# Performance work log

Measured on AMD Instinct MI355X. Metric: run time of the kernel, lower is better.

The kernel has to match this reference:

```python
import jax, jax.numpy as jnp
import numpy as np

B, S, F = 4, 2048, 512
H, DK, DV, FILT = 8, 64, 64, 512

def setup_inputs() -> dict:
    key = jax.random.key(0)
    ks = jax.random.split(key, 11)
    sc_in = 1.0 / np.sqrt(F)
    sc_o = 1.0 / np.sqrt(H * DV)
    return {
        "x_q": jax.random.normal(ks[0], (B, S, F), jnp.float32),
        "x_k": jax.random.normal(ks[1], (B, S, F), jnp.float32),
        "x_v": jax.random.normal(ks[2], (B, S, F), jnp.float32),
        "Wq": jax.random.normal(ks[3], (H, F, DK), jnp.float32) * sc_in,
        "bq": jax.random.normal(ks[4], (H, DK), jnp.float32) * 0.01,
        "Wk": jax.random.normal(ks[5], (H, F, DK), jnp.float32) * sc_in,
        "bk": jax.random.normal(ks[6], (H, DK), jnp.float32) * 0.01,
        "Wv": jax.random.normal(ks[7], (H, F, DV), jnp.float32) * sc_in,
        "bv": jax.random.normal(ks[8], (H, DV), jnp.float32) * 0.01,
        "Wo": jax.random.normal(ks[9], (H * DV, FILT), jnp.float32) * sc_o,
        "bo": jax.random.normal(ks[10], (FILT,), jnp.float32) * 0.01,
    }

def reference(x_q, x_k, x_v, Wq, bq, Wk, bk, Wv, bv, Wo, bo):
    d_k = Wq.shape[-1]
    # per-head Dense projections, batched over heads: [B,H,S,dk/dv]
    q = jnp.einsum("bsf,hfk->bhsk", x_q, Wq) + bq[:, None, :]
    k = jnp.einsum("bsf,hfk->bhsk", x_k, Wk) + bk[:, None, :]
    v = jnp.einsum("bsf,hfv->bhsv", x_v, Wv) + bv[:, None, :]
    # scaled dot-product attention (scale by 1/sqrt(d_k) as in map_fn)
    scores = jnp.einsum("bhsk,bhtk->bhst", q, k) / jnp.sqrt(jnp.asarray(d_k, q.dtype))
    attn = jax.nn.softmax(scores, axis=-1)
    out = jnp.einsum("bhst,bhtv->bhsv", attn, v)
    # concat heads along feature dim -> [B,S,H*DV], then output linear
    bsz, h, s, dv = out.shape
    concat = out.transpose(0, 2, 1, 3).reshape(bsz, s, h * dv)
    return concat @ Wo + bo
```

## Files before the change

kernel.cpp:

```cpp
#include <hip/hip_runtime.h>

#define B_    4
#define S_    2048
#define H_    8
#define M_    (B_ * S_)

typedef __bf16    bf16_t;
typedef _Float16  f16_t;
typedef __bf16   bf16x8 __attribute__((ext_vector_type(8)));
typedef __bf16   bf16x4 __attribute__((ext_vector_type(4)));
typedef _Float16 f16x8  __attribute__((ext_vector_type(8)));
typedef float    f32x16 __attribute__((ext_vector_type(16)));

union B8 { uint4 u; bf16x8 v; bf16_t e[8]; };
union B4 { uint2 u; bf16x4 v; bf16_t e[4]; };
union H8 { uint4 u; f16x8  v; f16_t  e[8]; };
union H4 { uint2 u; f16_t  e[4]; };

#define QSCALE 0.1803368801111204f

typedef const __attribute__((address_space(1))) unsigned int ga_u32;
typedef __attribute__((address_space(3))) unsigned int       ls_u32;
__device__ __forceinline__ void g2l16(const void* g, void* l) {
    __builtin_amdgcn_global_load_lds((ga_u32*)g, (ls_u32*)l, 16, 0, 0);
}

__global__ __launch_bounds__(256) void cast_x(
    const float* __restrict__ xq, const float* __restrict__ xk,
    const float* __restrict__ xv,
    bf16_t* __restrict__ dq, bf16_t* __restrict__ dk, bf16_t* __restrict__ dv)
{
    const int z = blockIdx.y;
    const float* src = z == 0 ? xq : z == 1 ? xk : xv;
    bf16_t*      dst = z == 0 ? dq : z == 1 ? dk : dv;
    const size_t base = (size_t)blockIdx.x * 4096 + threadIdx.x * 4;
    #pragma unroll
    for (int k = 0; k < 4; ++k) {
        const size_t i = base + (size_t)k * 1024;
        float4 v = *(const float4*)(src + i);
        B4 o;
        o.e[0] = (bf16_t)v.x; o.e[1] = (bf16_t)v.y;
        o.e[2] = (bf16_t)v.z; o.e[3] = (bf16_t)v.w;
        *(uint2*)(dst + i) = o.u;
    }
}

__global__ __launch_bounds__(256) void convert_weights(
    const float* __restrict__ w0, const float* __restrict__ w1,
    const float* __restrict__ w2, const float* __restrict__ wo,
    bf16_t* __restrict__ t0, bf16_t* __restrict__ t1,
    bf16_t* __restrict__ t2, f16_t* __restrict__ wot)
{
    __shared__ float T[64][65];
    const int z   = blockIdx.z;
    const int k0  = blockIdx.x * 64;
    const int tid = threadIdx.x;
    const int row = tid & 63, q4 = tid >> 6;

    if (z < 3) {
        const float* W  = z == 0 ? w0 : z == 1 ? w1 : w2;
        bf16_t*      Wt = z == 0 ? t0 : z == 1 ? t1 : t2;
        const int h = blockIdx.y;
        const float* Wh = W + (size_t)h * 512 * 64;
        #pragma unroll
        for (int i = 0; i < 4; ++i) {
            int fq = q4 * 4 + i;
            float4 v = *(const float4*)(Wh + (size_t)(k0 + row) * 64 + fq * 4);
            T[row][fq * 4 + 0] = v.x; T[row][fq * 4 + 1] = v.y;
            T[row][fq * 4 + 2] = v.z; T[row][fq * 4 + 3] = v.w;
        }
        __syncthreads();
        bf16_t* Wth = Wt + (size_t)h * 64 * 512;
        #pragma unroll
        for (int i = 0; i < 4; ++i) {
            int kq = q4 * 4 + i;
            B4 o;
            #pragma unroll
            for (int j = 0; j < 4; ++j) o.e[j] = (bf16_t)T[kq * 4 + j][row];
            *(uint2*)(Wth + (size_t)row * 512 + k0 + kq * 4) = o.u;
        }
    } else {
        const int n0 = blockIdx.y * 64;
        #pragma unroll
        for (int i = 0; i < 4; ++i) {
            int fq = q4 * 4 + i;
            float4 v = *(const float4*)(wo + (size_t)(k0 + row) * 512 + n0 + fq * 4);
            T[row][fq * 4 + 0] = v.x; T[row][fq * 4 + 1] = v.y;
            T[row][fq * 4 + 2] = v.z; T[row][fq * 4 + 3] = v.w;
        }
        __syncthreads();
        #pragma unroll
        for (int i = 0; i < 4; ++i) {
            int kq = q4 * 4 + i;
            H4 o;
            #pragma unroll
            for (int j = 0; j < 4; ++j) o.e[j] = (f16_t)T[kq * 4 + j][row];
            *(uint2*)(wot + (size_t)(n0 + row) * 512 + k0 + kq * 4) = o.u;
        }
    }
}

__global__ __launch_bounds__(256) void proj_tiled(
    const bf16_t* __restrict__ xq, const bf16_t* __restrict__ xk,
    const bf16_t* __restrict__ xv,
    const bf16_t* __restrict__ Wtq, const bf16_t* __restrict__ Wtk,
    const bf16_t* __restrict__ Wtv,
    const float* __restrict__ bq, const float* __restrict__ bk,
    const float* __restrict__ bv,
    bf16_t* __restrict__ Qb, bf16_t* __restrict__ Kb, bf16_t* __restrict__ Vt)
{
    __shared__ char sm[34816];
    bf16_t* As = (bf16_t*)sm;
    bf16_t* Bs = As + 128 * 64;

    const int z = blockIdx.z;
    const bf16_t* X    = z == 0 ? xq  : z == 1 ? xk  : xv;
    const bf16_t* Wt   = z == 0 ? Wtq : z == 1 ? Wtk : Wtv;
    const float*  bias = z == 0 ? bq  : z == 1 ? bk  : bv;

    const int tid  = threadIdx.x;
    const int wave = tid >> 6, lane = tid & 63;
    const int l31  = lane & 31, half = lane >> 5;
    const int m0   = blockIdx.x * 128;
    const int n0   = blockIdx.y * 128;
    const int mw   = (wave & 1) * 64;
    const int nw   = (wave >> 1) * 64;

    const int srow = lane >> 3;
    const int scol = (lane & 7) * 16;

    f32x16 acc[2][2];
    #pragma unroll
    for (int mt = 0; mt < 2; ++mt)
        #pragma unroll
        for (int nt = 0; nt < 2; ++nt)
            #pragma unroll
            for (int i = 0; i < 16; ++i) acc[mt][nt][i] = 0.0f;

    for (int k0 = 0; k0 < 512; k0 += 64) {
        __syncthreads();
        #pragma unroll
        for (int i = 0; i < 4; ++i) {
            const int inst = wave * 4 + i;
            const int row  = inst * 8 + srow;
            g2l16((const char*)X  + ((size_t)(m0 + row) * 512 + k0) * 2 + scol,
                  sm + inst * 1024);
            g2l16((const char*)Wt + ((size_t)(n0 + row) * 512 + k0) * 2 + scol,
                  sm + 16384 + inst * 1024);
        }
        __syncthreads();

        #pragma unroll
        for (int kc = 0; kc < 4; ++kc) {
            B8 a0, a1, b0, b1;
            a0.u = *(const uint4*)&As[(mw + l31)      * 64 + kc * 16 + half * 8];
            a1.u = *(const uint4*)&As[(mw + 32 + l31) * 64 + kc * 16 + half * 8];
            b0.u = *(const uint4*)&Bs[(nw + l31)      * 64 + kc * 16 + half * 8];
            b1.u = *(const uint4*)&Bs[(nw + 32 + l31) * 64 + kc * 16 + half * 8];
            acc[0][0] = __builtin_amdgcn_mfma_f32_32x32x16_bf16(a0.v, b0.v, acc[0][0], 0, 0, 0);
            acc[0][1] = __builtin_amdgcn_mfma_f32_32x32x16_bf16(a0.v, b1.v, acc[0][1], 0, 0, 0);
            acc[1][0] = __builtin_amdgcn_mfma_f32_32x32x16_bf16(a1.v, b0.v, acc[1][0], 0, 0, 0);
            acc[1][1] = __builtin_amdgcn_mfma_f32_32x32x16_bf16(a1.v, b1.v, acc[1][1], 0, 0, 0);
        }
    }

    if (z <= 1) {
        const float sc_ = (z == 0) ? QSCALE : 1.0f;
        bf16_t* Out = (z == 0) ? Qb : Kb;
        #pragma unroll
        for (int mt = 0; mt < 2; ++mt)
            #pragma unroll
            for (int nt = 0; nt < 2; ++nt) {
                int n = n0 + nw + nt * 32 + l31;
                float bv_ = bias[n];
                #pragma unroll
                for (int r = 0; r < 16; ++r) {
                    int m = m0 + mw + mt * 32 + (r & 3) + 8 * (r >> 2) + 4 * half;
                    Out[(size_t)m * 512 + n] = (bf16_t)((acc[mt][nt][r] + bv_) * sc_);
                }
            }
    } else {
        const int b  = m0 >> 11;
        const int sb = m0 & 2047;
        __syncthreads();
        #pragma unroll
        for (int mt = 0; mt < 2; ++mt)
            #pragma unroll
            for (int nt = 0; nt < 2; ++nt) {
                const int nl  = nw + nt * 32 + l31;
                const float bv_ = bias[n0 + nl];
                #pragma unroll
                for (int r = 0; r < 16; r += 2) {
                    const int ml = mw + mt * 32 + (r & 3) + 8 * (r >> 2) + 4 * half;
                    union { unsigned u; bf16_t e[2]; } pk;
                    pk.e[0] = (bf16_t)(acc[mt][nt][r]     + bv_);
                    pk.e[1] = (bf16_t)(acc[mt][nt][r + 1] + bv_);
                    *(unsigned*)(sm + nl * 272 + ml * 2) = pk.u;
                }
            }
        __syncthreads();
        const int dl16 = tid >> 4;
        const int cc   = tid & 15;
        #pragma unroll
        for (int p = 0; p < 8; ++p) {
            const int d_l = p * 16 + dl16;
            const int ng  = n0 + d_l;
            const int h   = ng >> 6, dd = ng & 63;
            uint4 val = *(const uint4*)(sm + d_l * 272 + cc * 16);
            *(uint4*)(Vt + ((size_t)((b * 8 + h) * 64 + dd)) * 2048 + sb + cc * 8) = val;
        }
    }
}

__global__ __launch_bounds__(512) void attn_mfma(
    const bf16_t* __restrict__ Q, const bf16_t* __restrict__ K,
    const bf16_t* __restrict__ Vt, f16_t* __restrict__ O)
{
    __shared__ char smraw[36864];
    bf16_t* KsBuf = (bf16_t*)smraw;
    bf16_t* VsBuf = KsBuf + 2 * 64 * 72;

    const int bh  = blockIdx.y;
    const int b   = bh >> 3, h = bh & 7;
    const int q0  = blockIdx.x * 128;
    const int tid = threadIdx.x;
    const int wave = tid >> 6, lane = tid & 63;
    const int l31 = lane & 31, half = lane >> 5;
    const int qsub = wave & 3, ksplit = wave >> 2;

    bf16x8 qf[4];
    {
        const bf16_t* qp = Q + ((size_t)(b * S_ + q0 + qsub * 32 + l31)) * 512 + h * 64 + half * 8;
        #pragma unroll
        for (int ks = 0; ks < 4; ++ks) {
            B8 t; t.u = *(const uint4*)(qp + ks * 16);
            qf[ks] = t.v;
        }
    }

    f32x16 o0, o1;
    #pragma unroll
    for (int i = 0; i < 16; ++i) { o0[i] = 0.0f; o1[i] = 0.0f; }
    float l_i = 0.0f;

    const bf16_t* Kbase = K + ((size_t)b * S_) * 512 + h * 64;
    const bf16_t* Vbase = Vt + ((size_t)bh * 64) * 2048;

    const int sbuf = tid >> 8;
    const int p    = tid & 255;
    const int kr = p >> 3, kc8 = p & 7;
    const int vd = p >> 2, vj = p & 3;
    const int kqmap[4] = {0, 2, 1, 3};
    const int vkq = kqmap[vj];
    bf16_t* KsS = KsBuf + sbuf * (64 * 72);
    bf16_t* VsS = VsBuf + sbuf * (64 * 72);
    const bf16_t* KsC = KsBuf + ksplit * (64 * 72);
    const bf16_t* VsC = VsBuf + ksplit * (64 * 72);

    uint4 kreg0, kreg1;
    uint2 vreg[4];
    {
        const int tb = sbuf * 1024;
        kreg0 = *(const uint4*)(Kbase + (size_t)(tb + kr) * 512 + kc8 * 8);
        kreg1 = *(const uint4*)(Kbase + (size_t)(tb + kr + 32) * 512 + kc8 * 8);
        #pragma unroll
        for (int g = 0; g < 4; ++g)
            vreg[g] = *(const uint2*)(Vbase + (size_t)vd * 2048 + tb + g * 16 + vkq * 4);
    }

    for (int t0 = 0; t0 < 1024; t0 += 64) {
        __syncthreads();
        *(uint4*)&KsS[kr * 72 + kc8 * 8]        = kreg0;
        *(uint4*)&KsS[(kr + 32) * 72 + kc8 * 8] = kreg1;
        #pragma unroll
        for (int g = 0; g < 4; ++g)
            *(uint2*)&VsS[vd * 72 + g * 16 + vj * 4] = vreg[g];
        __syncthreads();

        if (t0 + 64 < 1024) {
            const int tb = sbuf * 1024 + t0 + 64;
            kreg0 = *(const uint4*)(Kbase + (size_t)(tb + kr) * 512 + kc8 * 8);
            kreg1 = *(const uint4*)(Kbase + (size_t)(tb + kr + 32) * 512 + kc8 * 8);
            #pragma unroll
            for (int g = 0; g < 4; ++g)
                vreg[g] = *(const uint2*)(Vbase + (size_t)vd * 2048 + tb + g * 16 + vkq * 4);
        }

        f32x16 s0, s1;
        #pragma unroll
        for (int i = 0; i < 16; ++i) { s0[i] = 0.0f; s1[i] = 0.0f; }
        #pragma unroll
        for (int ks = 0; ks < 4; ++ks) {
            B8 k0, k1;
            k0.u = *(const uint4*)(&KsC[l31 * 72 + ks * 16 + half * 8]);
            k1.u = *(const uint4*)(&KsC[(32 + l31) * 72 + ks * 16 + half * 8]);
            s0 = __builtin_amdgcn_mfma_f32_32x32x16_bf16(k0.v, qf[ks], s0, 0, 0, 0);
            s1 = __builtin_amdgcn_mfma_f32_32x32x16_bf16(k1.v, qf[ks], s1, 0, 0, 0);
        }

        float ls = 0.0f;
        #pragma unroll
        for (int r = 0; r < 16; ++r) {
            s0[r] = __builtin_amdgcn_exp2f(s0[r]); ls += s0[r];
            s1[r] = __builtin_amdgcn_exp2f(s1[r]); ls += s1[r];
        }
        l_i += ls;

        B8 pf[4];
        #pragma unroll
        for (int j = 0; j < 8; ++j) {
            pf[0].e[j] = (bf16_t)s0[j];
            pf[1].e[j] = (bf16_t)s0[8 + j];
            pf[2].e[j] = (bf16_t)s1[j];
            pf[3].e[j] = (bf16_t)s1[8 + j];
        }

        #pragma unroll
        for (int c = 0; c < 4; ++c) {
            B8 va, vb;
            va.u = *(const uint4*)(&VsC[l31 * 72 + c * 16 + half * 8]);
            vb.u = *(const uint4*)(&VsC[(32 + l31) * 72 + c * 16 + half * 8]);
            o0 = __builtin_amdgcn_mfma_f32_32x32x16_bf16(va.v, pf[c].v, o0, 0, 0, 0);
            o1 = __builtin_amdgcn_mfma_f32_32x32x16_bf16(vb.v, pf[c].v, o1, 0, 0, 0);
        }
    }

    l_i += __shfl_xor(l_i, 32);
    __syncthreads();
    float* co = (float*)smraw;
    float* cl = co + 4 * 32 * 68;
    if (ksplit == 1) {
        float* reg = co + qsub * (32 * 68);
        #pragma unroll
        for (int r = 0; r < 16; ++r) {
            reg[r * 68 + lane]        = o0[r];
            reg[(16 + r) * 68 + lane] = o1[r];
        }
        cl[qsub * 64 + lane] = l_i;
    }
    __syncthreads();
    if (ksplit == 0) {
        float* reg = co + qsub * (32 * 68);
        float inv = 1.0f / (l_i + cl[qsub * 64 + lane]);
        f16_t* Ob = O + ((size_t)(b * S_ + q0 + qsub * 32 + l31)) * 512 + h * 64;
        #pragma unroll
        for (int g = 0; g < 4; ++g) {
            H4 a, c;
            #pragma unroll
            for (int j = 0; j < 4; ++j) {
                int r = g * 4 + j;
                a.e[j] = (f16_t)((o0[r] + reg[r * 68 + lane]) * inv);
                c.e[j] = (f16_t)((o1[r] + reg[(16 + r) * 68 + lane]) * inv);
            }
            int d = 8 * g + 4 * half;
            *(uint2*)(Ob + d)      = a.u;
            *(uint2*)(Ob + 32 + d) = c.u;
        }
    }
}

__global__ __launch_bounds__(256) void gemm_out_tiled(
    const f16_t* __restrict__ A, const f16_t* __restrict__ Wot,
    const float* __restrict__ bias, float* __restrict__ C)
{
    __shared__ f16_t As[64 * 72];
    __shared__ f16_t Bs[64 * 72];

    const int tid  = threadIdx.x;
    const int wave = tid >> 6, lane = tid & 63;
    const int l31  = lane & 31, half = lane >> 5;
    const int m0   = blockIdx.x * 64;
    const int n0   = blockIdx.y * 64;
    const int mw   = (wave & 1) * 32;
    const int nw   = (wave >> 1) * 32;

    const int sr  = tid >> 2;
    const int so  = (tid & 3) * 16;

    uint4 pA0, pA1, pB0, pB1;
    {
        const f16_t* ap = A   + (size_t)(m0 + sr) * 512 + so;
        const f16_t* bp = Wot + (size_t)(n0 + sr) * 512 + so;
        pA0 = *(const uint4*)(ap); pA1 = *(const uint4*)(ap + 8);
        pB0 = *(const uint4*)(bp); pB1 = *(const uint4*)(bp + 8);
    }

    f32x16 acc;
    #pragma unroll
    for (int i = 0; i < 16; ++i) acc[i] = 0.0f;

    for (int k0 = 0; k0 < 512; k0 += 64) {
        __syncthreads();
        *(uint4*)&As[sr * 72 + so]     = pA0;
        *(uint4*)&As[sr * 72 + so + 8] = pA1;
        *(uint4*)&Bs[sr * 72 + so]     = pB0;
        *(uint4*)&Bs[sr * 72 + so + 8] = pB1;
        __syncthreads();
        if (k0 + 64 < 512) {
            const f16_t* ap = A   + (size_t)(m0 + sr) * 512 + k0 + 64 + so;
            const f16_t* bp = Wot + (size_t)(n0 + sr) * 512 + k0 + 64 + so;
            pA0 = *(const uint4*)(ap); pA1 = *(const uint4*)(ap + 8);
            pB0 = *(const uint4*)(bp); pB1 = *(const uint4*)(bp + 8);
        }

        #pragma unroll
        for (int kc = 0; kc < 4; ++kc) {
            H8 a, b;
            a.u = *(const uint4*)&As[(mw + l31) * 72 + kc * 16 + half * 8];
            b.u = *(const uint4*)&Bs[(nw + l31) * 72 + kc * 16 + half * 8];
            acc = __builtin_amdgcn_mfma_f32_32x32x16_f16(a.v, b.v, acc, 0, 0, 0);
        }
    }

    const int n = n0 + nw + l31;
    const float bias0 = bias[n];
    #pragma unroll
    for (int r = 0; r < 16; ++r) {
        int m = m0 + mw + (r & 3) + 8 * (r >> 2) + 4 * half;
        C[(size_t)m * 512 + n] = acc[r] + bias0;
    }
}

extern "C" void kernel_launch(void* const* d_in, const int* in_sizes, int n_in,
                              void* d_out, int out_size, void* d_ws, size_t ws_size,
                              hipStream_t stream)
{
    const float* x_q = (const float*)d_in[0];
    const float* x_k = (const float*)d_in[1];
    const float* x_v = (const float*)d_in[2];
    const float* Wq  = (const float*)d_in[3];
    const float* bq  = (const float*)d_in[4];
    const float* Wk  = (const float*)d_in[5];
    const float* bk  = (const float*)d_in[6];
    const float* Wv  = (const float*)d_in[7];
    const float* bv  = (const float*)d_in[8];
    const float* Wo  = (const float*)d_in[9];
    const float* bo  = (const float*)d_in[10];
    float* out = (float*)d_out;

    char* W = (char*)d_ws;
    bf16_t* Wtq = (bf16_t*)W;
    bf16_t* Wtk = Wtq + (size_t)8 * 64 * 512;
    bf16_t* Wtv = Wtk + (size_t)8 * 64 * 512;
    f16_t*  Wot = (f16_t*)(Wtv + (size_t)8 * 64 * 512);
    bf16_t* Qb  = (bf16_t*)(Wot + (size_t)512 * 512);
    bf16_t* Kb  = Qb + (size_t)M_ * 512;
    bf16_t* Vt  = Kb + (size_t)M_ * 512;
    f16_t*  AO  = (f16_t*)(Vt + (size_t)M_ * 512);

    bf16_t* Xqb = (bf16_t*)out;
    bf16_t* Xkb = Xqb + (size_t)M_ * 512;
    bf16_t* Xvb = (bf16_t*)AO;

    cast_x<<<dim3(1024, 3), 256, 0, stream>>>(x_q, x_k, x_v, Xqb, Xkb, Xvb);

    convert_weights<<<dim3(8, 8, 4), 256, 0, stream>>>(
        Wq, Wk, Wv, Wo, Wtq, Wtk, Wtv, Wot);

    proj_tiled<<<dim3(64, 4, 3), 256, 0, stream>>>(
        Xqb, Xkb, Xvb, Wtq, Wtk, Wtv, bq, bk, bv, Qb, Kb, Vt);

    attn_mfma<<<dim3(S_ / 128, B_ * H_), 512, 0, stream>>>(Qb, Kb, Vt, AO);

    gemm_out_tiled<<<dim3(128, 8), 256, 0, stream>>>(AO, Wot, bo, out);
}
```

Before: 202.8 us.

## Double-buffer K/V register prefetch, remap blocks to head-major order, add MFMA priority

After: 199.1 us. No clear change (-1.8%).

```diff
diff --git a/kernel.cpp b/kernel.cpp
--- a/kernel.cpp
+++ b/kernel.cpp
@@ -220,9 +220,10 @@
     bf16_t* KsBuf = (bf16_t*)smraw;
     bf16_t* VsBuf = KsBuf + 2 * 64 * 72;
 
-    const int bh  = blockIdx.y;
+    const int lin = (int)(blockIdx.x + gridDim.x * blockIdx.y);
+    const int bh  = ((lin >> 7) << 3) + (lin & 7);
+    const int q0  = ((lin >> 3) & 15) * 128;
     const int b   = bh >> 3, h = bh & 7;
-    const int q0  = blockIdx.x * 128;
     const int tid = threadIdx.x;
     const int wave = tid >> 6, lane = tid & 63;
     const int l31 = lane & 31, half = lane >> 5;
@@ -257,38 +258,45 @@
     const bf16_t* KsC = KsBuf + ksplit * (64 * 72);
     const bf16_t* VsC = VsBuf + ksplit * (64 * 72);
 
-    uint4 kreg0, kreg1;
-    uint2 vreg[4];
-    {
-        const int tb = sbuf * 1024;
-        kreg0 = *(const uint4*)(Kbase + (size_t)(tb + kr) * 512 + kc8 * 8);
-        kreg1 = *(const uint4*)(Kbase + (size_t)(tb + kr + 32) * 512 + kc8 * 8);
-        #pragma unroll
-        for (int g = 0; g < 4; ++g)
-            vreg[g] = *(const uint2*)(Vbase + (size_t)vd * 2048 + tb + g * 16 + vkq * 4);
-    }
-
-    for (int t0 = 0; t0 < 1024; t0 += 64) {
-        __syncthreads();
-        *(uint4*)&KsS[kr * 72 + kc8 * 8]        = kreg0;
-        *(uint4*)&KsS[(kr + 32) * 72 + kc8 * 8] = kreg1;
-        #pragma unroll
-        for (int g = 0; g < 4; ++g)
-            *(uint2*)&VsS[vd * 72 + g * 16 + vj * 4] = vreg[g];
-        __syncthreads();
-
-        if (t0 + 64 < 1024) {
-            const int tb = sbuf * 1024 + t0 + 64;
-            kreg0 = *(const uint4*)(Kbase + (size_t)(tb + kr) * 512 + kc8 * 8);
-            kreg1 = *(const uint4*)(Kbase + (size_t)(tb + kr + 32) * 512 + kc8 * 8);
-            #pragma unroll
-            for (int g = 0; g < 4; ++g)
-                vreg[g] = *(const uint2*)(Vbase + (size_t)vd * 2048 + tb + g * 16 + vkq * 4);
+    uint4 k0A, k1A, k0B, k1B;
+    uint2 vA[4], vB[4];
+
+#define LOADSET(K0, K1, VV, TB) do {                                          \
+        K0 = *(const uint4*)(Kbase + (size_t)((TB) + kr) * 512 + kc8 * 8);    \
+        K1 = *(const uint4*)(Kbase + (size_t)((TB) + kr + 32) * 512 + kc8 * 8);\
+        _Pragma("unroll")                                                     \
+        for (int g = 0; g < 4; ++g)                                           \
+            VV[g] = *(const uint2*)(Vbase + (size_t)vd * 2048 + (TB) + g * 16 + vkq * 4); \
+    } while (0)
+
+#define WRITESET(K0, K1, VV) do {                                             \
+        *(uint4*)&KsS[kr * 72 + kc8 * 8]        = K0;                         \
+        *(uint4*)&KsS[(kr + 32) * 72 + kc8 * 8] = K1;                         \
+        _Pragma("unroll")                                                     \
+        for (int g = 0; g < 4; ++g)                                           \
+            *(uint2*)&VsS[vd * 72 + g * 16 + vj * 4] = VV[g];                 \
+    } while (0)
+
+    LOADSET(k0A, k1A, vA, sbuf * 1024);
+    LOADSET(k0B, k1B, vB, sbuf * 1024 + 64);
+
+    #pragma unroll
+    for (int it = 0; it < 16; ++it) {
+        __syncthreads();
+        if ((it & 1) == 0) WRITESET(k0A, k1A, vA);
+        else               WRITESET(k0B, k1B, vB);
+        __syncthreads();
+
+        if (it + 2 < 16) {
+            const int tb = sbuf * 1024 + it * 64 + 128;
+            if ((it & 1) == 0) LOADSET(k0A, k1A, vA, tb);
+            else               LOADSET(k0B, k1B, vB, tb);
         }
 
         f32x16 s0, s1;
         #pragma unroll
         for (int i = 0; i < 16; ++i) { s0[i] = 0.0f; s1[i] = 0.0f; }
+        __builtin_amdgcn_s_setprio(1);
         #pragma unroll
         for (int ks = 0; ks < 4; ++ks) {
             B8 k0, k1;
@@ -297,6 +305,7 @@
             s0 = __builtin_amdgcn_mfma_f32_32x32x16_bf16(k0.v, qf[ks], s0, 0, 0, 0);
             s1 = __builtin_amdgcn_mfma_f32_32x32x16_bf16(k1.v, qf[ks], s1, 0, 0, 0);
         }
+        __builtin_amdgcn_s_setprio(0);
 
         float ls = 0.0f;
         #pragma unroll
@@ -315,6 +324,7 @@
             pf[3].e[j] = (bf16_t)s1[8 + j];
         }
 
+        __builtin_amdgcn_s_setprio(1);
         #pragma unroll
         for (int c = 0; c < 4; ++c) {
             B8 va, vb;
@@ -323,7 +333,10 @@
             o0 = __builtin_amdgcn_mfma_f32_32x32x16_bf16(va.v, pf[c].v, o0, 0, 0, 0);
             o1 = __builtin_amdgcn_mfma_f32_32x32x16_bf16(vb.v, pf[c].v, o1, 0, 0, 0);
         }
-    }
+        __builtin_amdgcn_s_setprio(0);
+    }
+#undef LOADSET
+#undef WRITESET
 
     l_i += __shfl_xor(l_i, 32);
     __syncthreads();
```

## Process two query sub-tiles per wave in attention to reuse K/V tiles

Applied to the files above, without the earlier changes.

New measurement: 195.0 us. -3.8%, faster.

```diff
diff --git a/kernel.cpp b/kernel.cpp
--- a/kernel.cpp
+++ b/kernel.cpp
@@ -212,36 +212,37 @@
     }
 }
 
-__global__ __launch_bounds__(512) void attn_mfma(
+__global__ __launch_bounds__(512, 2) void attn_mfma(
     const bf16_t* __restrict__ Q, const bf16_t* __restrict__ K,
     const bf16_t* __restrict__ Vt, f16_t* __restrict__ O)
 {
-    __shared__ char smraw[36864];
+    __shared__ char smraw[71680];
     bf16_t* KsBuf = (bf16_t*)smraw;
     bf16_t* VsBuf = KsBuf + 2 * 64 * 72;
 
     const int bh  = blockIdx.y;
     const int b   = bh >> 3, h = bh & 7;
-    const int q0  = blockIdx.x * 128;
+    const int q0  = blockIdx.x * 256;
     const int tid = threadIdx.x;
     const int wave = tid >> 6, lane = tid & 63;
     const int l31 = lane & 31, half = lane >> 5;
     const int qsub = wave & 3, ksplit = wave >> 2;
 
-    bf16x8 qf[4];
+    bf16x8 qfA[4], qfB[4];
     {
-        const bf16_t* qp = Q + ((size_t)(b * S_ + q0 + qsub * 32 + l31)) * 512 + h * 64 + half * 8;
+        const bf16_t* qp = Q + ((size_t)(b * S_ + q0 + qsub * 64 + l31)) * 512 + h * 64 + half * 8;
         #pragma unroll
         for (int ks = 0; ks < 4; ++ks) {
-            B8 t; t.u = *(const uint4*)(qp + ks * 16);
-            qf[ks] = t.v;
-        }
-    }
-
-    f32x16 o0, o1;
+            B8 t;
+            t.u = *(const uint4*)(qp + ks * 16);              qfA[ks] = t.v;
+            t.u = *(const uint4*)(qp + 32 * 512 + ks * 16);   qfB[ks] = t.v;
+        }
+    }
+
+    f32x16 oA0, oA1, oB0, oB1;
     #pragma unroll
-    for (int i = 0; i < 16; ++i) { o0[i] = 0.0f; o1[i] = 0.0f; }
-    float l_i = 0.0f;
+    for (int i = 0; i < 16; ++i) { oA0[i] = 0.0f; oA1[i] = 0.0f; oB0[i] = 0.0f; oB1[i] = 0.0f; }
+    float lA = 0.0f, lB = 0.0f;
 
     const bf16_t* Kbase = K + ((size_t)b * S_) * 512 + h * 64;
     const bf16_t* Vbase = Vt + ((size_t)bh * 64) * 2048;
@@ -286,33 +287,41 @@
                 vreg[g] = *(const uint2*)(Vbase + (size_t)vd * 2048 + tb + g * 16 + vkq * 4);
         }
 
-        f32x16 s0, s1;
-        #pragma unroll
-        for (int i = 0; i < 16; ++i) { s0[i] = 0.0f; s1[i] = 0.0f; }
+        f32x16 s00, s01, s10, s11;
+        #pragma unroll
+        for (int i = 0; i < 16; ++i) { s00[i] = 0.0f; s01[i] = 0.0f; s10[i] = 0.0f; s11[i] = 0.0f; }
         #pragma unroll
         for (int ks = 0; ks < 4; ++ks) {
-            B8 k0, k1;
-            k0.u = *(const uint4*)(&KsC[l31 * 72 + ks * 16 + half * 8]);
-            k1.u = *(const uint4*)(&KsC[(32 + l31) * 72 + ks * 16 + half * 8]);
-            s0 = __builtin_amdgcn_mfma_f32_32x32x16_bf16(k0.v, qf[ks], s0, 0, 0, 0);
-            s1 = __builtin_amdgcn_mfma_f32_32x32x16_bf16(k1.v, qf[ks], s1, 0, 0, 0);
-        }
-
-        float ls = 0.0f;
+            B8 kk0, kk1;
+            kk0.u = *(const uint4*)(&KsC[l31 * 72 + ks * 16 + half * 8]);
+            kk1.u = *(const uint4*)(&KsC[(32 + l31) * 72 + ks * 16 + half * 8]);
+            s00 = __builtin_amdgcn_mfma_f32_32x32x16_bf16(kk0.v, qfA[ks], s00, 0, 0, 0);
+            s01 = __builtin_amdgcn_mfma_f32_32x32x16_bf16(kk0.v, qfB[ks], s01, 0, 0, 0);
+            s10 = __builtin_amdgcn_mfma_f32_32x32x16_bf16(kk1.v, qfA[ks], s10, 0, 0, 0);
+            s11 = __builtin_amdgcn_mfma_f32_32x32x16_bf16(kk1.v, qfB[ks], s11, 0, 0, 0);
+        }
+
+        float lsA = 0.0f, lsB = 0.0f;
         #pragma unroll
         for (int r = 0; r < 16; ++r) {
-            s0[r] = __builtin_amdgcn_exp2f(s0[r]); ls += s0[r];
-            s1[r] = __builtin_amdgcn_exp2f(s1[r]); ls += s1[r];
-        }
-        l_i += ls;
-
-        B8 pf[4];
+            s00[r] = __builtin_amdgcn_exp2f(s00[r]); lsA += s00[r];
+            s10[r] = __builtin_amdgcn_exp2f(s10[r]); lsA += s10[r];
+            s01[r] = __builtin_amdgcn_exp2f(s01[r]); lsB += s01[r];
+            s11[r] = __builtin_amdgcn_exp2f(s11[r]); lsB += s11[r];
+        }
+        lA += lsA; lB += lsB;
+
+        B8 pfA[4], pfB[4];
         #pragma unroll
         for (int j = 0; j < 8; ++j) {
-            pf[0].e[j] = (bf16_t)s0[j];
-            pf[1].e[j] = (bf16_t)s0[8 + j];
-            pf[2].e[j] = (bf16_t)s1[j];
-            pf[3].e[j] = (bf16_t)s1[8 + j];
+            pfA[0].e[j] = (bf16_t)s00[j];
+            pfA[1].e[j] = (bf16_t)s00[8 + j];
+            pfA[2].e[j] = (bf16_t)s10[j];
+            pfA[3].e[j] = (bf16_t)s10[8 + j];
+            pfB[0].e[j] = (bf16_t)s01[j];
+            pfB[1].e[j] = (bf16_t)s01[8 + j];
+            pfB[2].e[j] = (bf16_t)s11[j];
+            pfB[3].e[j] = (bf16_t)s11[8 + j];
         }
 
         #pragma unroll
@@ -320,41 +329,53 @@
             B8 va, vb;
             va.u = *(const uint4*)(&VsC[l31 * 72 + c * 16 + half * 8]);
             vb.u = *(const uint4*)(&VsC[(32 + l31) * 72 + c * 16 + half * 8]);
-            o0 = __builtin_amdgcn_mfma_f32_32x32x16_bf16(va.v, pf[c].v, o0, 0, 0, 0);
-            o1 = __builtin_amdgcn_mfma_f32_32x32x16_bf16(vb.v, pf[c].v, o1, 0, 0, 0);
-        }
-    }
-
-    l_i += __shfl_xor(l_i, 32);
+            oA0 = __builtin_amdgcn_mfma_f32_32x32x16_bf16(va.v, pfA[c].v, oA0, 0, 0, 0);
+            oA1 = __builtin_amdgcn_mfma_f32_32x32x16_bf16(vb.v, pfA[c].v, oA1, 0, 0, 0);
+            oB0 = __builtin_amdgcn_mfma_f32_32x32x16_bf16(va.v, pfB[c].v, oB0, 0, 0, 0);
+            oB1 = __builtin_amdgcn_mfma_f32_32x32x16_bf16(vb.v, pfB[c].v, oB1, 0, 0, 0);
+        }
+    }
+
+    lA += __shfl_xor(lA, 32);
+    lB += __shfl_xor(lB, 32);
     __syncthreads();
     float* co = (float*)smraw;
-    float* cl = co + 4 * 32 * 68;
+    float* cl = co + 4 * 64 * 68;
     if (ksplit == 1) {
-        float* reg = co + qsub * (32 * 68);
+        float* reg = co + qsub * (64 * 68);
         #pragma unroll
         for (int r = 0; r < 16; ++r) {
-            reg[r * 68 + lane]        = o0[r];
-            reg[(16 + r) * 68 + lane] = o1[r];
-        }
-        cl[qsub * 64 + lane] = l_i;
+            reg[r * 68 + lane]        = oA0[r];
+            reg[(16 + r) * 68 + lane] = oA1[r];
+            reg[(32 + r) * 68 + lane] = oB0[r];
+            reg[(48 + r) * 68 + lane] = oB1[r];
+        }
+        cl[qsub * 128 + lane]      = lA;
+        cl[qsub * 128 + 64 + lane] = lB;
     }
     __syncthreads();
     if (ksplit == 0) {
-        float* reg = co + qsub * (32 * 68);
-        float inv = 1.0f / (l_i + cl[qsub * 64 + lane]);
-        f16_t* Ob = O + ((size_t)(b * S_ + q0 + qsub * 32 + l31)) * 512 + h * 64;
+        float* reg = co + qsub * (64 * 68);
+        float invA = 1.0f / (lA + cl[qsub * 128 + lane]);
+        float invB = 1.0f / (lB + cl[qsub * 128 + 64 + lane]);
+        f16_t* ObA = O + ((size_t)(b * S_ + q0 + qsub * 64 + l31)) * 512 + h * 64;
+        f16_t* ObB = ObA + (size_t)32 * 512;
         #pragma unroll
         for (int g = 0; g < 4; ++g) {
-            H4 a, c;
+            H4 a, c, e, f;
             #pragma unroll
             for (int j = 0; j < 4; ++j) {
                 int r = g * 4 + j;
-                a.e[j] = (f16_t)((o0[r] + reg[r * 68 + lane]) * inv);
-                c.e[j] = (f16_t)((o1[r] + reg[(16 + r) * 68 + lane]) * inv);
+                a.e[j] = (f16_t)((oA0[r] + reg[r * 68 + lane])        * invA);
+                c.e[j] = (f16_t)((oA1[r] + reg[(16 + r) * 68 + lane]) * invA);
+                e.e[j] = (f16_t)((oB0[r] + reg[(32 + r) * 68 + lane]) * invB);
+                f.e[j] = (f16_t)((oB1[r] + reg[(48 + r) * 68 + lane]) * invB);
             }
             int d = 8 * g + 4 * half;
-            *(uint2*)(Ob + d)      = a.u;
-            *(uint2*)(Ob + 32 + d) = c.u;
+            *(uint2*)(ObA + d)      = a.u;
+            *(uint2*)(ObA + 32 + d) = c.u;
+            *(uint2*)(ObB + d)      = e.u;
+            *(uint2*)(ObB + 32 + d) = f.u;
         }
     }
 }
@@ -460,7 +481,7 @@
     proj_tiled<<<dim3(64, 4, 3), 256, 0, stream>>>(
         Xqb, Xkb, Xvb, Wtq, Wtk, Wtv, bq, bk, bv, Qb, Kb, Vt);
 
-    attn_mfma<<<dim3(S_ / 128, B_ * H_), 512, 0, stream>>>(Qb, Kb, Vt, AO);
+    attn_mfma<<<dim3(S_ / 256, B_ * H_), 512, 0, stream>>>(Qb, Kb, Vt, AO);
 
     gemm_out_tiled<<<dim3(128, 8), 256, 0, stream>>>(AO, Wot, bo, out);
 }
```
